# Optimization experiments

Measured on AMD Instinct MI355X. Metric: run time of the kernel, lower is better.

Reference implementation:

```python
import jax, jax.numpy as jnp
import numpy as np

ALPHA = 0.25


def setup_inputs() -> dict:
    key = jax.random.key(0)
    pos_seq = jax.random.normal(key, (64, 8192, 51), dtype=jnp.float32)
    return {"pos_seq": pos_seq}


def _ema(pos_seq, alpha):
    # out[0] = x[0]; out[t] = alpha*x[t] + (1-alpha)*out[t-1]
    x0 = pos_seq[:, 0]                      # (B, D)
    xs = jnp.swapaxes(pos_seq[:, 1:], 0, 1)  # (T-1, B, D) for scan over time

    def step(carry, x_t):
        y = alpha * x_t + (1.0 - alpha) * carry
        return y, y

    _, ys = jax.lax.scan(step, x0, xs)      # ys: (T-1, B, D)
    ys = jnp.swapaxes(ys, 0, 1)             # (B, T-1, D)
    return jnp.concatenate([pos_seq[:, :1], ys], axis=1)


def reference(pos_seq):
    return _ema(pos_seq, ALPHA)
```

## Files before the change

kernel.cpp:

```cpp
#include <hip/hip_runtime.h>


#define EMA_ALPHA 0.25f
#define EMA_BETA  0.75f
#define T_DIM 8192
#define C_DIM 51
#define CHUNK_L 64
#define HALO_H  48
#define NCHUNK (T_DIM / CHUNK_L)

__global__ __launch_bounds__(256, 8) void ema_kernel(const float* __restrict__ x,
                                                     float* __restrict__ y,
                                                     int total_threads) {
    int gid = blockIdx.x * blockDim.x + threadIdx.x;
    if (gid >= total_threads) return;

    int c = gid % C_DIM;
    int rest = gid / C_DIM;
    int chunk = rest % NCHUNK;
    int b = rest / NCHUNK;

    const size_t seq_base = (size_t)b * T_DIM * C_DIM + c;
    const float* __restrict__ xb = x + seq_base;
    float* __restrict__ yb = y + seq_base;

    const int t0 = chunk * CHUNK_L;
    const int th = t0 - HALO_H;

    int i0 = th < 0 ? 0 : th;
    float acc = xb[(size_t)i0 * C_DIM];
#pragma unroll
    for (int i = 1; i < HALO_H; ++i) {
        int ti = th + i;
        ti = ti < 0 ? 0 : ti;
        float xv = xb[(size_t)ti * C_DIM];
        acc = fmaf(EMA_ALPHA, xv, EMA_BETA * acc);
    }

#pragma unroll
    for (int j = 0; j < CHUNK_L; ++j) {
        const int t = t0 + j;
        float xv = xb[(size_t)t * C_DIM];
        acc = fmaf(EMA_ALPHA, xv, EMA_BETA * acc);
        __builtin_nontemporal_store(acc, &yb[(size_t)t * C_DIM]);
    }
}

extern "C" void kernel_launch(void* const* d_in, const int* in_sizes, int n_in,
                              void* d_out, int out_size, void* d_ws, size_t ws_size,
                              hipStream_t stream) {
    const float* x = (const float*)d_in[0];
    float* y = (float*)d_out;

    int B = in_sizes[0] / (T_DIM * C_DIM);
    int total = B * NCHUNK * C_DIM;
    int block = 256;
    int grid = (total + block - 1) / block;

    ema_kernel<<<grid, block, 0, stream>>>(x, y, total);
}
```

Baseline: 211.0 us.

## Stage EMA chunks in shared memory with vectorized coalesced loads and stores

Each block now loads a 176-row tile (128 output rows plus a 48-row halo) of one batch into LDS with float4 loads. 204 threads scan 32-row subchunks, each warming up over a 48-row halo from LDS, and write results back into the tile. The tile is then written out with vectorized nontemporal stores. This replaces the strided per-thread 4-byte global accesses and reduces halo re-reads from 48/64 to 48/128 per output row. In exchange it uses about 35KB of LDS per block, leaves about 20% of threads idle during the scan, and adds three barriers.

```diff
diff --git a/kernel.cpp b/kernel.cpp
--- a/kernel.cpp
+++ b/kernel.cpp
@@ -1,48 +1,83 @@
 #include <hip/hip_runtime.h>
 
 
-#define EMA_ALPHA 0.25f
-#define EMA_BETA  0.75f
+typedef float vfloat4 __attribute__((ext_vector_type(4)));
+
 #define T_DIM 8192
 #define C_DIM 51
-#define CHUNK_L 64
-#define HALO_H  48
-#define NCHUNK (T_DIM / CHUNK_L)
+#define L_ROWS 128
+#define H_ROWS 48
+#define TILE_ROWS (L_ROWS + H_ROWS)
+#define TILE_ELEMS (TILE_ROWS * C_DIM)
+#define OUT_ELEMS (L_ROWS * C_DIM)
+#define SUB_LEN 32
+#define NSUB 4
+#define NCHUNK (T_DIM / L_ROWS)
 
-__global__ __launch_bounds__(256, 8) void ema_kernel(const float* __restrict__ x,
-                                                     float* __restrict__ y,
-                                                     int total_threads) {
-    int gid = blockIdx.x * blockDim.x + threadIdx.x;
-    if (gid >= total_threads) return;
+__global__ __launch_bounds__(256, 4) void ema_kernel(const float* __restrict__ x,
+                                                     float* __restrict__ y) {
+    __shared__ float tile[TILE_ELEMS];
 
-    int c = gid % C_DIM;
-    int rest = gid / C_DIM;
-    int chunk = rest % NCHUNK;
-    int b = rest / NCHUNK;
+    const int tid = threadIdx.x;
+    const int chunk = blockIdx.x % NCHUNK;
+    const int b = blockIdx.x / NCHUNK;
+    const size_t plane = (size_t)b * ((size_t)T_DIM * C_DIM);
+    const int t0 = chunk * L_ROWS;
+    const int start_f = (t0 - H_ROWS) * C_DIM;
 
-    const size_t seq_base = (size_t)b * T_DIM * C_DIM + c;
-    const float* __restrict__ xb = x + seq_base;
-    float* __restrict__ yb = y + seq_base;
+    const float* __restrict__ xp = x + plane;
 
-    const int t0 = chunk * CHUNK_L;
-    const int th = t0 - HALO_H;
+    if (chunk != 0) {
+        for (int j = tid; j < TILE_ELEMS / 4; j += 256) {
+            vfloat4 v = *(const vfloat4*)(xp + start_f + 4 * j);
+            *(vfloat4*)(&tile[4 * j]) = v;
+        }
+    } else {
+        for (int j = tid; j < TILE_ELEMS / 4; j += 256) {
+            int e = start_f + 4 * j;
+            if (e >= 0) {
+                *(vfloat4*)(&tile[4 * j]) = *(const vfloat4*)(xp + e);
+            } else {
+                vfloat4 v;
+#pragma unroll
+                for (int k = 0; k < 4; ++k) {
+                    int c = (e + k + H_ROWS * C_DIM) % C_DIM;
+                    v[k] = xp[c];
+                }
+                *(vfloat4*)(&tile[4 * j]) = v;
+            }
+        }
+    }
+    __syncthreads();
 
-    int i0 = th < 0 ? 0 : th;
-    float acc = xb[(size_t)i0 * C_DIM];
+    const int c = tid % C_DIM;
+    const int sub = tid / C_DIM;
+    const bool active = (tid < NSUB * C_DIM);
+    float acc = 0.0f;
+    if (active) {
+        const int tr = sub * SUB_LEN;
+        acc = tile[tr * C_DIM + c];
 #pragma unroll
-    for (int i = 1; i < HALO_H; ++i) {
-        int ti = th + i;
-        ti = ti < 0 ? 0 : ti;
-        float xv = xb[(size_t)ti * C_DIM];
-        acc = fmaf(EMA_ALPHA, xv, EMA_BETA * acc);
+        for (int i = 1; i < H_ROWS; ++i)
+            acc = fmaf(0.25f, tile[(tr + i) * C_DIM + c], 0.75f * acc);
     }
+    __syncthreads();
 
+    if (active) {
+        const int base = (H_ROWS + sub * SUB_LEN) * C_DIM + c;
 #pragma unroll
-    for (int j = 0; j < CHUNK_L; ++j) {
-        const int t = t0 + j;
-        float xv = xb[(size_t)t * C_DIM];
-        acc = fmaf(EMA_ALPHA, xv, EMA_BETA * acc);
-        __builtin_nontemporal_store(acc, &yb[(size_t)t * C_DIM]);
+        for (int i = 0; i < SUB_LEN; ++i) {
+            float xv = tile[base + i * C_DIM];
+            acc = fmaf(0.25f, xv, 0.75f * acc);
+            tile[base + i * C_DIM] = acc;
+        }
+    }
+    __syncthreads();
+
+    float* __restrict__ yp = y + plane + (size_t)t0 * C_DIM;
+    for (int j = tid; j < OUT_ELEMS / 4; j += 256) {
+        vfloat4 v = *(const vfloat4*)(&tile[H_ROWS * C_DIM + 4 * j]);
+        __builtin_nontemporal_store(v, (vfloat4*)(yp + 4 * j));
     }
 }
 
@@ -53,9 +88,6 @@
     float* y = (float*)d_out;
 
     int B = in_sizes[0] / (T_DIM * C_DIM);
-    int total = B * NCHUNK * C_DIM;
-    int block = 256;
-    int grid = (total + block - 1) / block;
-
-    ema_kernel<<<grid, block, 0, stream>>>(x, y, total);
+    int grid = B * NCHUNK;
+    ema_kernel<<<grid, 256, 0, stream>>>(x, y);
 }
```

After: 190.6 us. -9.7%, faster.
